# Kernel optimization log

Measured on AMD Instinct MI355X. Metric: run time of the kernel, lower is better.

The kernel has to match this reference:

```python
import jax, jax.numpy as jnp
import numpy as np

B, L, D, V = 2048, 32, 256, 100000  # batch, sentence length, embed dim, vocab
KW = 3  # kernel_width (forced to 3 by the module's shape arithmetic)


def conv_h(x, w, b):
    """1-channel conv over the seq axis, kernel (3,1), pad 2 -> length L+2. x:(B,L,D), w:(3,)."""
    xp = jnp.pad(x, ((0, 0), (2, 2), (0, 0)))
    L_out = x.shape[1] + 2
    out = w[0] * xp[:, 0:L_out] + w[1] * xp[:, 1:L_out + 1] + w[2] * xp[:, 2:L_out + 2]
    return out + b


def avgpool3(x):
    """avg_pool2d kernel (3,1) stride 1 along seq axis. (B,L+2,D) -> (B,L,D)."""
    return (x[:, :-2] + x[:, 1:-1] + x[:, 2:]) / 3.0


def conv3d_21(x, w, b):
    """Conv3d kernel (2,3,1), pad (0,2,0). x:(B,2,L,D), w:(2,3) -> (B,L+2,D)."""
    xp = jnp.pad(x, ((0, 0), (0, 0), (2, 2), (0, 0)))
    L_out = x.shape[2] + 2
    out = jnp.zeros((x.shape[0], L_out, x.shape[3]), dtype=x.dtype)
    for d0 in range(2):
        for k in range(3):
            out = out + w[d0, k] * xp[:, d0, k:k + L_out]
    return out + b


def euclid_attention(a, b):
    """A[k,i,j] = 1/(1 + ||a[k,i]-b[k,j]||_2), computed via the matmul cdist trick."""
    a2 = jnp.sum(a * a, axis=-1)  # (B,La)
    b2 = jnp.sum(b * b, axis=-1)  # (B,Lb)
    d2 = a2[:, :, None] + b2[:, None, :] - 2.0 * jnp.einsum('bid,bjd->bij', a, b)
    d = jnp.sqrt(jnp.maximum(d2, 0.0))
    return 1.0 / (1.0 + d)


def setup_inputs() -> dict:
    key = jax.random.key(0)
    ks = jax.random.split(key, 16)
    inp = {
        'sentence1': jax.random.randint(ks[0], (B, L), 0, V),
        'sentence2': jax.random.randint(ks[1], (B, L), 0, V),
        'embed': jax.random.normal(ks[2], (V, D), dtype=jnp.float32) * 0.05,
        'c1w': jax.random.normal(ks[3], (KW,), dtype=jnp.float32) * 0.3,
        'c1b': jax.random.normal(ks[4], (), dtype=jnp.float32) * 0.05,
        'c2w': jax.random.normal(ks[5], (KW,), dtype=jnp.float32) * 0.3,
        'c2b': jax.random.normal(ks[6], (), dtype=jnp.float32) * 0.05,
        'c3w': jax.random.normal(ks[7], (2, KW), dtype=jnp.float32) * 0.3,
        'c3b': jax.random.normal(ks[8], (), dtype=jnp.float32) * 0.05,
        'W0': jax.random.normal(ks[9], (L, D), dtype=jnp.float32),
        'W1': jax.random.normal(ks[10], (L, D), dtype=jnp.float32),
        'fw1': jax.random.normal(ks[11], (2 * D, 64), dtype=jnp.float32) * 0.05,
        'fb1': jnp.zeros((64,), dtype=jnp.float32),
        'fw2': jax.random.normal(ks[12], (64, 2), dtype=jnp.float32) * 0.1,
        'fb2': jnp.zeros((2,), dtype=jnp.float32),
    }
    return inp


def reference(sentence1, sentence2, embed, c1w, c1b, c2w, c2b, c3w, c3b, W0, W1, fw1, fb1, fw2, fb2):
    e1 = embed[sentence1]                      # (B,L,D)
    e2 = embed[sentence2]
    rep1 = avgpool3(conv_h(e1, c1w, c1b))      # (B,L,D)
    rep2 = avgpool3(conv_h(e2, c1w, c1b))
    A1 = euclid_attention(rep1, rep2)          # (B,L,L)
    att1 = jnp.einsum('bij,jd->bid', A1, W0)   # (B,L,D)
    att2 = jnp.einsum('bij,jd->bid', A1, W1)
    c1 = conv3d_21(jnp.stack([rep1, att1], axis=1), c3w, c3b)  # (B,L+2,D)
    c2 = conv3d_21(jnp.stack([rep2, att2], axis=1), c3w, c3b)
    A2 = euclid_attention(c1, c2)              # (B,L+2,L+2)
    col = jnp.sum(A2, axis=2)                  # (B,L+2)
    row = jnp.sum(A2, axis=1)
    ca1 = avgpool3(c1 * col[:, :, None])       # (B,L,D)
    ca2 = avgpool3(c2 * row[:, :, None])
    v1 = jnp.mean(conv_h(ca1, c2w, c2b), axis=1)  # (B,D)
    v2 = jnp.mean(conv_h(ca2, c2w, c2b), axis=1)
    h = jnp.tanh(jnp.concatenate([v1, v2], axis=1) @ fw1 + fb1)
    logits = h @ fw2 + fb2                     # (B,2)
    return jax.nn.softmax(logits, axis=0)      # faithful: original Softmax(dim=0)
```

## Files before the change

### kernel.cpp

```cpp
#include <hip/hip_runtime.h>
#include <math.h>

#define NB 2048
#define LL 32
#define DD 256
#define LP 34
#define SRH 264
#define SA 35

typedef unsigned short u16;
typedef short bf8 __attribute__((ext_vector_type(8)));
typedef float f32x4 __attribute__((ext_vector_type(4)));
typedef float vf2 __attribute__((ext_vector_type(2)));

__device__ __forceinline__ float bfu(u16 h) { return __uint_as_float(((unsigned)h) << 16); }
__device__ __forceinline__ u16 f2bf(float f) {
    unsigned u = __float_as_uint(f);
    u += 0x7fffu + ((u >> 16) & 1u);
    return (u16)(u >> 16);
}
__device__ __forceinline__ unsigned cvt_pk_bf(float lo, float hi) {
    unsigned r;
    asm("v_cvt_pk_bf16_f32 %0, %1, %2" : "=v"(r) : "v"(lo), "v"(hi));
    return r;
}

__device__ __forceinline__ f32x4 gram8(const u16* __restrict__ A, const u16* __restrict__ B) {
    f32x4 acc = {0.f, 0.f, 0.f, 0.f};
    #pragma unroll
    for (int ks = 0; ks < 8; ++ks) {
        const bf8 a = *(const bf8*)(A + ks * 32);
        const bf8 b = *(const bf8*)(B + ks * 32);
        acc = __builtin_amdgcn_mfma_f32_16x16x32_bf16(a, b, acc, 0, 0, 0);
    }
    return acc;
}

__device__ static const signed char TB2[8][4] = {
    {0,0,1,0}, {0,0,1,16}, {0,16,1,0}, {0,16,1,16},
    {0,0,0,0}, {0,16,0,16}, {1,0,1,0}, {1,16,1,16}};

__device__ static const signed char TB5[15][4] = {
    {0,0,0,0}, {0,16,0,16}, {0,18,0,18}, {1,0,1,0}, {1,16,1,16}, {1,18,1,18},
    {0,0,1,0},  {0,0,1,16},  {0,0,1,18},
    {0,16,1,0}, {0,16,1,16}, {0,16,1,18},
    {0,18,1,0}, {0,18,1,16}, {0,18,1,18}};

__global__ __launch_bounds__(256)
void pack_w(const float* __restrict__ W0, const float* __restrict__ W1, u16* __restrict__ wp)
{
    const int t = blockIdx.x * 256 + threadIdx.x;
    const int lane = t & 63, nt = (t >> 6) & 15, wsel = t >> 10;
    const float* W = wsel ? W1 : W0;
    const int col = nt * 16 + (lane & 15);
    const int k0 = (lane >> 4) * 8;
    unsigned d[4];
    #pragma unroll
    for (int q = 0; q < 4; ++q) {
        const u16 lo = f2bf(W[(size_t)(k0 + 2 * q) * DD + col]);
        const u16 hi = f2bf(W[(size_t)(k0 + 2 * q + 1) * DD + col]);
        d[q] = (unsigned)lo | ((unsigned)hi << 16);
    }
    uint4 u; u.x = d[0]; u.y = d[1]; u.z = d[2]; u.w = d[3];
    ((uint4*)wp)[t] = u;
}

__global__ __launch_bounds__(256, 4)
void abcnn_fused(const int* __restrict__ s1, const int* __restrict__ s2,
                 const float* __restrict__ embed,
                 const float* __restrict__ c1w, const float* __restrict__ c1b,
                 const float* __restrict__ c2w, const float* __restrict__ c2b,
                 const float* __restrict__ c3w, const float* __restrict__ c3b,
                 const float* __restrict__ fw1, const float* __restrict__ fb1,
                 const float* __restrict__ fw2, const float* __restrict__ fb2,
                 const u16* __restrict__ wpack, float* __restrict__ lgts)
{
    __shared__ __align__(16) u16 RC[2][LP][SRH];
    __shared__ float AU[LP * SA];
    __shared__ float nrm[2][LP];

    const int b    = blockIdx.x;
    const int tid  = threadIdx.x;
    const int lane = tid & 63;
    const int wv   = tid >> 6;
    const int c15  = lane & 15;
    const int q4x  = (lane >> 4) * 4;
    const int ko   = (lane >> 4) * 8;

    {
        const float w0 = c1w[0], w1 = c1w[1], w2 = c1w[2], bb = c1b[0];
        const float gm2 = w0 * (1.f/3.f);
        const float gm1 = (w0 + w1) * (1.f/3.f);
        const float g0  = (w0 + w1 + w2) * (1.f/3.f);
        const float gp1 = (w1 + w2) * (1.f/3.f);
        const float gp2 = w2 * (1.f/3.f);
        const int s  = __builtin_amdgcn_readfirstlane(tid >> 7);
        const int dp = tid & 127;
        const int* sent = (s ? s2 : s1) + b * LL;
        int sv[LL];
        #pragma unroll
        for (int j = 0; j < LL; ++j) sv[j] = sent[j];
        #pragma unroll
        for (int half = 0; half < 2; ++half) {
            const int j0 = half * 16;
            vf2 x[20];
            #pragma unroll
            for (int i = 0; i < 20; ++i) {
                const int rr = j0 - 2 + i;
                if (rr >= 0 && rr < LL)
                    x[i] = *(const vf2*)(embed + (size_t)sv[rr] * DD + 2 * dp);
                else
                    x[i] = (vf2){0.f, 0.f};
            }
            #pragma unroll
            for (int j = 0; j < 16; ++j) {
                vf2 acc = {bb, bb};
                acc += gm2 * x[j];
                acc += gm1 * x[j + 1];
                acc += g0  * x[j + 2];
                acc += gp1 * x[j + 3];
                acc += gp2 * x[j + 4];
                *(unsigned*)&RC[s][j0 + j][2 * dp] = cvt_pk_bf(acc.x, acc.y);
            }
        }
    }
    __syncthreads();

    {
        f32x4 h2[2];
        __builtin_amdgcn_s_setprio(1);
        #pragma unroll
        for (int k = 0; k < 2; ++k) {
            const int t  = wv * 2 + k;
            const int sa = TB2[t][0], oa = TB2[t][1], sb = TB2[t][2], ob = TB2[t][3];
            const f32x4 G = gram8(&RC[sa][oa + c15][ko], &RC[sb][ob + c15][ko]);
            h2[k] = G;
            if (t >= 4 && (c15 >> 2) == (lane >> 4)) {
                const int r = c15 & 3;
                const float dv = (r == 0) ? G[0] : (r == 1) ? G[1] : (r == 2) ? G[2] : G[3];
                nrm[sa][oa + c15] = dv;
            }
        }
        __builtin_amdgcn_s_setprio(0);
        __syncthreads();
        #pragma unroll
        for (int k = 0; k < 2; ++k) {
            const int t = wv * 2 + k;
            if (t < 4) {
                const int oa = TB2[t][1], ob = TB2[t][3];
                const f32x4 G = h2[k];
                #pragma unroll
                for (int r = 0; r < 4; ++r) {
                    const int i = oa + q4x + r, j = ob + c15;
                    const float d2 = nrm[0][i] + nrm[1][j] - 2.f * G[r];
                    AU[i * SA + j] = 1.f / (1.f + sqrtf(fmaxf(d2, 0.f)));
                }
            }
        }
    }
    __syncthreads();

    {
        const float cw10 = c3w[3], cw11 = c3w[4], cw12 = c3w[5];
        const float cw00 = c3w[0], cw01 = c3w[1], cw02 = c3w[2], cb3 = c3b[0];
        bf8 afr[3];
        #pragma unroll
        for (int rq = 0; rq < 3; ++rq) {
            const int ro = (rq == 0) ? 0 : (rq == 1) ? 16 : 18;
            const int i = ro + c15;
            bf8 af;
            #pragma unroll
            for (int j = 0; j < 8; ++j) {
                const int m = ko + j;
                float acc = 0.f;
                if (i >= 2)           acc += cw10 * AU[(i - 2) * SA + m];
                if (i >= 1 && i < 33) acc += cw11 * AU[(i - 1) * SA + m];
                if (i < 32)           acc += cw12 * AU[i * SA + m];
                af[j] = (short)f2bf(acc);
            }
            afr[rq] = af;
        }
        __builtin_amdgcn_s_setprio(1);
        #pragma unroll
        for (int wsel = 0; wsel < 2; ++wsel) {
            #pragma unroll
            for (int nidx = 0; nidx < 4; ++nidx) {
                const int n = wv + 4 * nidx;
                const int dcol = n * 16 + c15;
                const bf8 w = *(const bf8*)(wpack + (size_t)((wsel * 16 + n) * 64 + lane) * 8);
                #pragma unroll
                for (int rqd = 0; rqd < 3; ++rqd) {
                    const int rq = 2 - rqd;
                    const int ro = (rq == 0) ? 0 : (rq == 1) ? 16 : 18;
                    const int i0 = ro + q4x;
                    const f32x4 z = {0.f, 0.f, 0.f, 0.f};
                    f32x4 d4 = __builtin_amdgcn_mfma_f32_16x16x32_bf16(afr[rq], w, z, 0, 0, 0);
                    float tt[6];
                    #pragma unroll
                    for (int q2 = 0; q2 < 6; ++q2) {
                        const int rr = i0 - 2 + q2;
                        tt[q2] = (rr >= 0 && rr < LL) ? bfu(RC[wsel][rr][dcol]) : 0.f;
                    }
                    #pragma unroll
                    for (int r = 0; r < 4; ++r)
                        d4[r] += cb3 + cw00 * tt[r] + cw01 * tt[r + 1] + cw02 * tt[r + 2];
                    const unsigned p01 = cvt_pk_bf(d4[0], d4[1]);
                    const unsigned p23 = cvt_pk_bf(d4[2], d4[3]);
                    if (rq < 2) {
                        RC[wsel][i0    ][dcol] = (u16)p01;
                        RC[wsel][i0 + 1][dcol] = (u16)(p01 >> 16);
                        RC[wsel][i0 + 2][dcol] = (u16)p23;
                        RC[wsel][i0 + 3][dcol] = (u16)(p23 >> 16);
                    } else if (q4x == 12) {
                        RC[wsel][32][dcol] = (u16)p23;
                        RC[wsel][33][dcol] = (u16)(p23 >> 16);
                    }
                }
            }
        }
        __builtin_amdgcn_s_setprio(0);
    }
    __syncthreads();

    {
        f32x4 h5[4];
        __builtin_amdgcn_s_setprio(1);
        #pragma unroll
        for (int k = 0; k < 4; ++k) {
            const int t = wv + 4 * k;
            if (t < 15) {
                const int sa = TB5[t][0], oa = TB5[t][1], sb = TB5[t][2], ob = TB5[t][3];
                const f32x4 G = gram8(&RC[sa][oa + c15][ko], &RC[sb][ob + c15][ko]);
                h5[k] = G;
                if (t < 6 && (c15 >> 2) == (lane >> 4)) {
                    const int r = c15 & 3;
                    const float dv = (r == 0) ? G[0] : (r == 1) ? G[1] : (r == 2) ? G[2] : G[3];
                    nrm[sa][oa + c15] = dv;
                }
            }
        }
        __builtin_amdgcn_s_setprio(0);
        __syncthreads();
        #pragma unroll
        for (int k = 0; k < 4; ++k) {
            const int t = wv + 4 * k;
            if (t >= 6 && t < 15) {
                const int oa = TB5[t][1], ob = TB5[t][3];
                const f32x4 G = h5[k];
                #pragma unroll
                for (int r = 0; r < 4; ++r) {
                    const int i = oa + q4x + r, j = ob + c15;
                    const float d2 = nrm[0][i] + nrm[1][j] - 2.f * G[r];
                    AU[i * SA + j] = 1.f / (1.f + sqrtf(fmaxf(d2, 0.f)));
                }
            }
        }
    }
    __syncthreads();

    {
        const float S2 = c2w[0] + c2w[1] + c2w[2];
        const float sc = S2 * (1.f / 102.f);
        float p6 = 0.f;
        if (tid < 68) {
            const bool isCol = tid < 34;
            const int p = isCol ? tid : tid - 34;
            float ssum = 0.f;
            for (int q = 0; q < LP; ++q) ssum += AU[isCol ? (p * SA + q) : (q * SA + p)];
            const float cnt = (p == 0 || p == 33) ? 1.f : ((p == 1 || p == 32) ? 2.f : 3.f);
            p6 = ssum * cnt * sc;
        }
        __syncthreads();
        if (tid < 68) AU[tid] = p6;
    }
    __syncthreads();

    {
        const float cb2 = c2b[0];
        float v1 = cb2, v2 = cb2;
        #pragma unroll
        for (int p = 0; p < LP; ++p) {
            v1 += AU[p]      * bfu(RC[0][p][tid]);
            v2 += AU[34 + p] * bfu(RC[1][p][tid]);
        }
        AU[68 + tid]       = v1;
        AU[68 + 256 + tid] = v2;
    }
    __syncthreads();

    {
        const int u = tid & 63, sg = tid >> 6;
        const float* vv = &AU[68];
        const float* fp = fw1 + (size_t)(sg * 128) * 64 + u;
        float part = 0.f;
        for (int t = 0; t < 128; ++t) part += vv[sg * 128 + t] * fp[(size_t)t * 64];
        AU[580 + tid] = part;
    }
    __syncthreads();
    if (tid < 64) {
        const float hsum = AU[580 + tid] + AU[644 + tid] + AU[708 + tid] + AU[772 + tid] + fb1[tid];
        AU[836 + tid] = tanhf(hsum);
    }
    __syncthreads();
    if (tid < 2) {
        float lg = fb2[tid];
        for (int u2 = 0; u2 < 64; ++u2) lg += AU[836 + u2] * fw2[u2 * 2 + tid];
        lgts[tid * NB + b] = lg;
    }
}

__global__ __launch_bounds__(1024)
void softmax_dim0(const float* __restrict__ lgts, float* __restrict__ out)
{
    __shared__ float red[17];
    const int tid = threadIdx.x;
    for (int c = 0; c < 2; ++c) {
        const float x0 = lgts[c * NB + tid];
        const float x1 = lgts[c * NB + 1024 + tid];
        float m = fmaxf(x0, x1);
        #pragma unroll
        for (int off = 32; off >= 1; off >>= 1) m = fmaxf(m, __shfl_xor(m, off));
        if ((tid & 63) == 0) red[tid >> 6] = m;
        __syncthreads();
        if (tid == 0) { float t = red[0]; for (int i = 1; i < 16; ++i) t = fmaxf(t, red[i]); red[16] = t; }
        __syncthreads();
        m = red[16];
        const float e0 = expf(x0 - m), e1 = expf(x1 - m);
        float s = e0 + e1;
        #pragma unroll
        for (int off = 32; off >= 1; off >>= 1) s += __shfl_xor(s, off);
        if ((tid & 63) == 0) red[tid >> 6] = s;
        __syncthreads();
        if (tid == 0) { float t = 0.f; for (int i = 0; i < 16; ++i) t += red[i]; red[16] = t; }
        __syncthreads();
        const float inv = 1.f / red[16];
        out[(size_t)tid * 2 + c]          = e0 * inv;
        out[(size_t)(1024 + tid) * 2 + c] = e1 * inv;
        __syncthreads();
    }
}

extern "C" void kernel_launch(void* const* d_in, const int* in_sizes, int n_in,
                              void* d_out, int out_size, void* d_ws, size_t ws_size,
                              hipStream_t stream)
{
    (void)in_sizes; (void)n_in; (void)out_size; (void)ws_size;
    const int*   s1  = (const int*)  d_in[0];
    const int*   s2  = (const int*)  d_in[1];
    const float* emb = (const float*)d_in[2];
    const float* c1w = (const float*)d_in[3];
    const float* c1b = (const float*)d_in[4];
    const float* c2w = (const float*)d_in[5];
    const float* c2b = (const float*)d_in[6];
    const float* c3w = (const float*)d_in[7];
    const float* c3b = (const float*)d_in[8];
    const float* fw1 = (const float*)d_in[11];
    const float* fb1 = (const float*)d_in[12];
    const float* fw2 = (const float*)d_in[13];
    const float* fb2 = (const float*)d_in[14];
    const float* W0  = (const float*)d_in[9];
    const float* W1  = (const float*)d_in[10];
    u16*   wpack = (u16*)d_ws;
    float* lgts  = (float*)((char*)d_ws + 32768);
    float* out   = (float*)d_out;

    pack_w<<<dim3(8), dim3(256), 0, stream>>>(W0, W1, wpack);
    abcnn_fused<<<dim3(NB), dim3(256), 0, stream>>>(s1, s2, emb, c1w, c1b, c2w, c2b,
                                                    c3w, c3b, fw1, fb1, fw2, fb2,
                                                    wpack, lgts);
    softmax_dim0<<<dim3(1), dim3(1024), 0, stream>>>(lgts, out);
}
```

Before: 66.57 us.

## Double block to 512 threads and split each stage across eight waves

The fused per-sample kernel now launches 512 threads instead of 256, and every stage is re-partitioned so each wave does half the previous work. This covers the embedding conv halves, the gram tiles, the W0/W1 MFMA selection, the pooled reductions and the fw1 partial sums. The aim is more independent waves in flight per sample to hide gather and LDS latency, with fewer serial iterations per wave. The launch bound changes from (256,4) to (512,8), which tightens the per-thread register budget and may cause spills in the register-heavy embedding stage.

```diff
diff --git a/kernel.cpp b/kernel.cpp
--- a/kernel.cpp
+++ b/kernel.cpp
@@ -65,7 +65,7 @@
     ((uint4*)wp)[t] = u;
 }
 
-__global__ __launch_bounds__(256, 4)
+__global__ __launch_bounds__(512, 8)
 void abcnn_fused(const int* __restrict__ s1, const int* __restrict__ s2,
                  const float* __restrict__ embed,
                  const float* __restrict__ c1w, const float* __restrict__ c1b,
@@ -94,67 +94,54 @@
         const float g0  = (w0 + w1 + w2) * (1.f/3.f);
         const float gp1 = (w1 + w2) * (1.f/3.f);
         const float gp2 = w2 * (1.f/3.f);
-        const int s  = __builtin_amdgcn_readfirstlane(tid >> 7);
-        const int dp = tid & 127;
+        const int s    = __builtin_amdgcn_readfirstlane((tid >> 7) & 1);
+        const int half = __builtin_amdgcn_readfirstlane(tid >> 8);
+        const int dp   = tid & 127;
         const int* sent = (s ? s2 : s1) + b * LL;
         int sv[LL];
         #pragma unroll
         for (int j = 0; j < LL; ++j) sv[j] = sent[j];
-        #pragma unroll
-        for (int half = 0; half < 2; ++half) {
-            const int j0 = half * 16;
-            vf2 x[20];
+        const int j0 = half * 16;
+        vf2 x[20];
+        #pragma unroll
+        for (int i = 0; i < 20; ++i) {
+            const int rr = j0 - 2 + i;
+            if (rr >= 0 && rr < LL)
+                x[i] = *(const vf2*)(embed + (size_t)sv[rr] * DD + 2 * dp);
+            else
+                x[i] = (vf2){0.f, 0.f};
+        }
+        #pragma unroll
+        for (int j = 0; j < 16; ++j) {
+            vf2 acc = {bb, bb};
+            acc += gm2 * x[j];
+            acc += gm1 * x[j + 1];
+            acc += g0  * x[j + 2];
+            acc += gp1 * x[j + 3];
+            acc += gp2 * x[j + 4];
+            *(unsigned*)&RC[s][j0 + j][2 * dp] = cvt_pk_bf(acc.x, acc.y);
+        }
+    }
+    __syncthreads();
+
+    {
+        const int t  = wv;
+        const int sa = TB2[t][0], oa = TB2[t][1], sb = TB2[t][2], ob = TB2[t][3];
+        __builtin_amdgcn_s_setprio(1);
+        const f32x4 G = gram8(&RC[sa][oa + c15][ko], &RC[sb][ob + c15][ko]);
+        __builtin_amdgcn_s_setprio(0);
+        if (t >= 4 && (c15 >> 2) == (lane >> 4)) {
+            const int r = c15 & 3;
+            const float dv = (r == 0) ? G[0] : (r == 1) ? G[1] : (r == 2) ? G[2] : G[3];
+            nrm[sa][oa + c15] = dv;
+        }
+        __syncthreads();
+        if (t < 4) {
             #pragma unroll
-            for (int i = 0; i < 20; ++i) {
-                const int rr = j0 - 2 + i;
-                if (rr >= 0 && rr < LL)
-                    x[i] = *(const vf2*)(embed + (size_t)sv[rr] * DD + 2 * dp);
-                else
-                    x[i] = (vf2){0.f, 0.f};
-            }
-            #pragma unroll
-            for (int j = 0; j < 16; ++j) {
-                vf2 acc = {bb, bb};
-                acc += gm2 * x[j];
-                acc += gm1 * x[j + 1];
-                acc += g0  * x[j + 2];
-                acc += gp1 * x[j + 3];
-                acc += gp2 * x[j + 4];
-                *(unsigned*)&RC[s][j0 + j][2 * dp] = cvt_pk_bf(acc.x, acc.y);
-            }
-        }
-    }
-    __syncthreads();
-
-    {
-        f32x4 h2[2];
-        __builtin_amdgcn_s_setprio(1);
-        #pragma unroll
-        for (int k = 0; k < 2; ++k) {
-            const int t  = wv * 2 + k;
-            const int sa = TB2[t][0], oa = TB2[t][1], sb = TB2[t][2], ob = TB2[t][3];
-            const f32x4 G = gram8(&RC[sa][oa + c15][ko], &RC[sb][ob + c15][ko]);
-            h2[k] = G;
-            if (t >= 4 && (c15 >> 2) == (lane >> 4)) {
-                const int r = c15 & 3;
-                const float dv = (r == 0) ? G[0] : (r == 1) ? G[1] : (r == 2) ? G[2] : G[3];
-                nrm[sa][oa + c15] = dv;
-            }
-        }
-        __builtin_amdgcn_s_setprio(0);
-        __syncthreads();
-        #pragma unroll
-        for (int k = 0; k < 2; ++k) {
-            const int t = wv * 2 + k;
-            if (t < 4) {
-                const int oa = TB2[t][1], ob = TB2[t][3];
-                const f32x4 G = h2[k];
-                #pragma unroll
-                for (int r = 0; r < 4; ++r) {
-                    const int i = oa + q4x + r, j = ob + c15;
-                    const float d2 = nrm[0][i] + nrm[1][j] - 2.f * G[r];
-                    AU[i * SA + j] = 1.f / (1.f + sqrtf(fmaxf(d2, 0.f)));
-                }
+            for (int r = 0; r < 4; ++r) {
+                const int i = oa + q4x + r, j = ob + c15;
+                const float d2 = nrm[0][i] + nrm[1][j] - 2.f * G[r];
+                AU[i * SA + j] = 1.f / (1.f + sqrtf(fmaxf(d2, 0.f)));
             }
         }
     }
@@ -180,42 +167,41 @@
             }
             afr[rq] = af;
         }
+        const int wsel = wv >> 2;
+        const int nW   = wv & 3;
         __builtin_amdgcn_s_setprio(1);
         #pragma unroll
-        for (int wsel = 0; wsel < 2; ++wsel) {
+        for (int nidx = 0; nidx < 4; ++nidx) {
+            const int n = nW + 4 * nidx;
+            const int dcol = n * 16 + c15;
+            const bf8 w = *(const bf8*)(wpack + (size_t)((wsel * 16 + n) * 64 + lane) * 8);
             #pragma unroll
-            for (int nidx = 0; nidx < 4; ++nidx) {
-                const int n = wv + 4 * nidx;
-                const int dcol = n * 16 + c15;
-                const bf8 w = *(const bf8*)(wpack + (size_t)((wsel * 16 + n) * 64 + lane) * 8);
+            for (int rqd = 0; rqd < 3; ++rqd) {
+                const int rq = 2 - rqd;
+                const int ro = (rq == 0) ? 0 : (rq == 1) ? 16 : 18;
+                const int i0 = ro + q4x;
+                const f32x4 z = {0.f, 0.f, 0.f, 0.f};
+                f32x4 d4 = __builtin_amdgcn_mfma_f32_16x16x32_bf16(afr[rq], w, z, 0, 0, 0);
+                float tt[6];
                 #pragma unroll
-                for (int rqd = 0; rqd < 3; ++rqd) {
-                    const int rq = 2 - rqd;
-                    const int ro = (rq == 0) ? 0 : (rq == 1) ? 16 : 18;
-                    const int i0 = ro + q4x;
-                    const f32x4 z = {0.f, 0.f, 0.f, 0.f};
-                    f32x4 d4 = __builtin_amdgcn_mfma_f32_16x16x32_bf16(afr[rq], w, z, 0, 0, 0);
-                    float tt[6];
-                    #pragma unroll
-                    for (int q2 = 0; q2 < 6; ++q2) {
-                        const int rr = i0 - 2 + q2;
-                        tt[q2] = (rr >= 0 && rr < LL) ? bfu(RC[wsel][rr][dcol]) : 0.f;
-                    }
-                    #pragma unroll
-                    for (int r = 0; r < 4; ++r)
-                        d4[r] += cb3 + cw00 * tt[r] + cw01 * tt[r + 1] + cw02 * tt[r + 2];
-                    const unsigned p01 = cvt_pk_bf(d4[0], d4[1]);
-                    const unsigned p23 = cvt_pk_bf(d4[2], d4[3]);
-                    if (rq < 2) {
-                        RC[wsel][i0    ][dcol] = (u16)p01;
-                        RC[wsel][i0 + 1][dcol] = (u16)(p01 >> 16);
-                        RC[wsel][i0 + 2][dcol] = (u16)p23;
-                        RC[wsel][i0 + 3][dcol] = (u16)(p23 >> 16);
-                    } else if (q4x == 12) {
-                        RC[wsel][32][dcol] = (u16)p23;
-                        RC[wsel][33][dcol] = (u16)(p23 >> 16);
-                    }
+                for (int q2 = 0; q2 < 6; ++q2) {
+                    const int rr = i0 - 2 + q2;
+                    tt[q2] = (rr >= 0 && rr < LL) ? bfu(RC[wsel][rr][dcol]) : 0.f;
                 }
+                #pragma unroll
+                for (int r = 0; r < 4; ++r)
+                    d4[r] += cb3 + cw00 * tt[r] + cw01 * tt[r + 1] + cw02 * tt[r + 2];
+                const unsigned p01 = cvt_pk_bf(d4[0], d4[1]);
+                const unsigned p23 = cvt_pk_bf(d4[2], d4[3]);
+                if (rq < 2) {
+                    RC[wsel][i0    ][dcol] = (u16)p01;
+                    RC[wsel][i0 + 1][dcol] = (u16)(p01 >> 16);
+                    RC[wsel][i0 + 2][dcol] = (u16)p23;
+                    RC[wsel][i0 + 3][dcol] = (u16)(p23 >> 16);
+                } else if (q4x == 12) {
+                    RC[wsel][32][dcol] = (u16)p23;
+                    RC[wsel][33][dcol] = (u16)(p23 >> 16);
+                }
             }
         }
         __builtin_amdgcn_s_setprio(0);
@@ -223,11 +209,11 @@
     __syncthreads();
 
     {
-        f32x4 h5[4];
+        f32x4 h5[2];
         __builtin_amdgcn_s_setprio(1);
         #pragma unroll
-        for (int k = 0; k < 4; ++k) {
-            const int t = wv + 4 * k;
+        for (int k = 0; k < 2; ++k) {
+            const int t = wv * 2 + k;
             if (t < 15) {
                 const int sa = TB5[t][0], oa = TB5[t][1], sb = TB5[t][2], ob = TB5[t][3];
                 const f32x4 G = gram8(&RC[sa][oa + c15][ko], &RC[sb][ob + c15][ko]);
@@ -242,8 +228,8 @@
         __builtin_amdgcn_s_setprio(0);
         __syncthreads();
         #pragma unroll
-        for (int k = 0; k < 4; ++k) {
-            const int t = wv + 4 * k;
+        for (int k = 0; k < 2; ++k) {
+            const int t = wv * 2 + k;
             if (t >= 6 && t < 15) {
                 const int oa = TB5[t][1], ob = TB5[t][3];
                 const f32x4 G = h5[k];
@@ -277,34 +263,35 @@
 
     {
         const float cb2 = c2b[0];
-        float v1 = cb2, v2 = cb2;
-        #pragma unroll
-        for (int p = 0; p < LP; ++p) {
-            v1 += AU[p]      * bfu(RC[0][p][tid]);
-            v2 += AU[34 + p] * bfu(RC[1][p][tid]);
-        }
-        AU[68 + tid]       = v1;
-        AU[68 + 256 + tid] = v2;
+        const int side = tid >> 8;
+        const int d    = tid & 255;
+        float v = cb2;
+        #pragma unroll
+        for (int p = 0; p < LP; ++p)
+            v += AU[side * 34 + p] * bfu(RC[side][p][d]);
+        AU[68 + tid] = v;
     }
     __syncthreads();
 
     {
         const int u = tid & 63, sg = tid >> 6;
         const float* vv = &AU[68];
-        const float* fp = fw1 + (size_t)(sg * 128) * 64 + u;
+        const float* fp = fw1 + (size_t)(sg * 64) * 64 + u;
         float part = 0.f;
-        for (int t = 0; t < 128; ++t) part += vv[sg * 128 + t] * fp[(size_t)t * 64];
+        for (int t = 0; t < 64; ++t) part += vv[sg * 64 + t] * fp[(size_t)t * 64];
         AU[580 + tid] = part;
     }
     __syncthreads();
     if (tid < 64) {
-        const float hsum = AU[580 + tid] + AU[644 + tid] + AU[708 + tid] + AU[772 + tid] + fb1[tid];
-        AU[836 + tid] = tanhf(hsum);
+        float hsum = fb1[tid];
+        #pragma unroll
+        for (int q = 0; q < 8; ++q) hsum += AU[580 + q * 64 + tid];
+        AU[1092 + tid] = tanhf(hsum);
     }
     __syncthreads();
     if (tid < 2) {
         float lg = fb2[tid];
-        for (int u2 = 0; u2 < 64; ++u2) lg += AU[836 + u2] * fw2[u2 * 2 + tid];
+        for (int u2 = 0; u2 < 64; ++u2) lg += AU[1092 + u2] * fw2[u2 * 2 + tid];
         lgts[tid * NB + b] = lg;
     }
 }
@@ -365,7 +352,7 @@
     float* out   = (float*)d_out;
 
     pack_w<<<dim3(8), dim3(256), 0, stream>>>(W0, W1, wpack);
-    abcnn_fused<<<dim3(NB), dim3(256), 0, stream>>>(s1, s2, emb, c1w, c1b, c2w, c2b,
+    abcnn_fused<<<dim3(NB), dim3(512), 0, stream>>>(s1, s2, emb, c1w, c1b, c2w, c2b,
                                                     c3w, c3b, fw1, fb1, fw2, fb2,
                                                     wpack, lgts);
     softmax_dim0<<<dim3(1), dim3(1024), 0, stream>>>(lgts, out);
```

Measured after the change: 109.7 us. 64.7% more time.

## Process two batch items per block and prefetch next embedding gather during compute

Applied to the files above, without the earlier changes.

Each block now handles two batch items: it issues the embedding gather for the second item right after building the first item's representation, so the global loads overlap the attention, MFMA and classifier stages of the first item. The grid is halved to 1024 blocks. The cost is keeping 36 vf2 gathered values live in registers, which raises register pressure and may lower occupancy under the 4-blocks-per-CU launch bound.

```diff
diff --git a/kernel.cpp b/kernel.cpp
--- a/kernel.cpp
+++ b/kernel.cpp
@@ -65,6 +65,38 @@
     ((uint4*)wp)[t] = u;
 }
 
+__device__ __forceinline__ void gather_issue(const int* __restrict__ s1, const int* __restrict__ s2,
+                                             const float* __restrict__ embed, int b, int tid, vf2* x)
+{
+    const int s  = __builtin_amdgcn_readfirstlane(tid >> 7);
+    const int dp = tid & 127;
+    const int* sent = (s ? s2 : s1) + b * LL;
+    #pragma unroll
+    for (int i = 0; i < 36; ++i) {
+        const int rr = i - 2;
+        if (rr >= 0 && rr < LL)
+            x[i] = *(const vf2*)(embed + (size_t)sent[rr] * DD + 2 * dp);
+        else
+            x[i] = (vf2){0.f, 0.f};
+    }
+}
+
+__device__ __forceinline__ void write_rep(u16 (*RCs)[SRH], int tid, const vf2* x,
+                                          float gm2, float gm1, float g0, float gp1, float gp2, float bb)
+{
+    const int dp = tid & 127;
+    #pragma unroll
+    for (int j = 0; j < LL; ++j) {
+        vf2 acc = {bb, bb};
+        acc += gm2 * x[j];
+        acc += gm1 * x[j + 1];
+        acc += g0  * x[j + 2];
+        acc += gp1 * x[j + 3];
+        acc += gp2 * x[j + 4];
+        *(unsigned*)&RCs[j][2 * dp] = cvt_pk_bf(acc.x, acc.y);
+    }
+}
+
 __global__ __launch_bounds__(256, 4)
 void abcnn_fused(const int* __restrict__ s1, const int* __restrict__ s2,
                  const float* __restrict__ embed,
@@ -79,233 +111,214 @@
     __shared__ float AU[LP * SA];
     __shared__ float nrm[2][LP];
 
-    const int b    = blockIdx.x;
+    const int bid  = blockIdx.x;
     const int tid  = threadIdx.x;
     const int lane = tid & 63;
     const int wv   = tid >> 6;
     const int c15  = lane & 15;
     const int q4x  = (lane >> 4) * 4;
     const int ko   = (lane >> 4) * 8;
-
-    {
-        const float w0 = c1w[0], w1 = c1w[1], w2 = c1w[2], bb = c1b[0];
-        const float gm2 = w0 * (1.f/3.f);
-        const float gm1 = (w0 + w1) * (1.f/3.f);
-        const float g0  = (w0 + w1 + w2) * (1.f/3.f);
-        const float gp1 = (w1 + w2) * (1.f/3.f);
-        const float gp2 = w2 * (1.f/3.f);
-        const int s  = __builtin_amdgcn_readfirstlane(tid >> 7);
-        const int dp = tid & 127;
-        const int* sent = (s ? s2 : s1) + b * LL;
-        int sv[LL];
-        #pragma unroll
-        for (int j = 0; j < LL; ++j) sv[j] = sent[j];
-        #pragma unroll
-        for (int half = 0; half < 2; ++half) {
-            const int j0 = half * 16;
-            vf2 x[20];
-            #pragma unroll
-            for (int i = 0; i < 20; ++i) {
-                const int rr = j0 - 2 + i;
-                if (rr >= 0 && rr < LL)
-                    x[i] = *(const vf2*)(embed + (size_t)sv[rr] * DD + 2 * dp);
-                else
-                    x[i] = (vf2){0.f, 0.f};
-            }
-            #pragma unroll
-            for (int j = 0; j < 16; ++j) {
-                vf2 acc = {bb, bb};
-                acc += gm2 * x[j];
-                acc += gm1 * x[j + 1];
-                acc += g0  * x[j + 2];
-                acc += gp1 * x[j + 3];
-                acc += gp2 * x[j + 4];
-                *(unsigned*)&RC[s][j0 + j][2 * dp] = cvt_pk_bf(acc.x, acc.y);
-            }
-        }
-    }
-    __syncthreads();
-
-    {
-        f32x4 h2[2];
-        __builtin_amdgcn_s_setprio(1);
-        #pragma unroll
-        for (int k = 0; k < 2; ++k) {
-            const int t  = wv * 2 + k;
-            const int sa = TB2[t][0], oa = TB2[t][1], sb = TB2[t][2], ob = TB2[t][3];
-            const f32x4 G = gram8(&RC[sa][oa + c15][ko], &RC[sb][ob + c15][ko]);
-            h2[k] = G;
-            if (t >= 4 && (c15 >> 2) == (lane >> 4)) {
-                const int r = c15 & 3;
-                const float dv = (r == 0) ? G[0] : (r == 1) ? G[1] : (r == 2) ? G[2] : G[3];
-                nrm[sa][oa + c15] = dv;
-            }
-        }
-        __builtin_amdgcn_s_setprio(0);
-        __syncthreads();
-        #pragma unroll
-        for (int k = 0; k < 2; ++k) {
-            const int t = wv * 2 + k;
-            if (t < 4) {
-                const int oa = TB2[t][1], ob = TB2[t][3];
-                const f32x4 G = h2[k];
-                #pragma unroll
-                for (int r = 0; r < 4; ++r) {
-                    const int i = oa + q4x + r, j = ob + c15;
-                    const float d2 = nrm[0][i] + nrm[1][j] - 2.f * G[r];
-                    AU[i * SA + j] = 1.f / (1.f + sqrtf(fmaxf(d2, 0.f)));
-                }
-            }
-        }
-    }
-    __syncthreads();
-
-    {
-        const float cw10 = c3w[3], cw11 = c3w[4], cw12 = c3w[5];
-        const float cw00 = c3w[0], cw01 = c3w[1], cw02 = c3w[2], cb3 = c3b[0];
-        bf8 afr[3];
-        #pragma unroll
-        for (int rq = 0; rq < 3; ++rq) {
-            const int ro = (rq == 0) ? 0 : (rq == 1) ? 16 : 18;
-            const int i = ro + c15;
-            bf8 af;
-            #pragma unroll
-            for (int j = 0; j < 8; ++j) {
-                const int m = ko + j;
-                float acc = 0.f;
-                if (i >= 2)           acc += cw10 * AU[(i - 2) * SA + m];
-                if (i >= 1 && i < 33) acc += cw11 * AU[(i - 1) * SA + m];
-                if (i < 32)           acc += cw12 * AU[i * SA + m];
-                af[j] = (short)f2bf(acc);
-            }
-            afr[rq] = af;
-        }
-        __builtin_amdgcn_s_setprio(1);
-        #pragma unroll
-        for (int wsel = 0; wsel < 2; ++wsel) {
-            #pragma unroll
-            for (int nidx = 0; nidx < 4; ++nidx) {
-                const int n = wv + 4 * nidx;
-                const int dcol = n * 16 + c15;
-                const bf8 w = *(const bf8*)(wpack + (size_t)((wsel * 16 + n) * 64 + lane) * 8);
-                #pragma unroll
-                for (int rqd = 0; rqd < 3; ++rqd) {
-                    const int rq = 2 - rqd;
-                    const int ro = (rq == 0) ? 0 : (rq == 1) ? 16 : 18;
-                    const int i0 = ro + q4x;
-                    const f32x4 z = {0.f, 0.f, 0.f, 0.f};
-                    f32x4 d4 = __builtin_amdgcn_mfma_f32_16x16x32_bf16(afr[rq], w, z, 0, 0, 0);
-                    float tt[6];
-                    #pragma unroll
-                    for (int q2 = 0; q2 < 6; ++q2) {
-                        const int rr = i0 - 2 + q2;
-                        tt[q2] = (rr >= 0 && rr < LL) ? bfu(RC[wsel][rr][dcol]) : 0.f;
-                    }
-                    #pragma unroll
-                    for (int r = 0; r < 4; ++r)
-                        d4[r] += cb3 + cw00 * tt[r] + cw01 * tt[r + 1] + cw02 * tt[r + 2];
-                    const unsigned p01 = cvt_pk_bf(d4[0], d4[1]);
-                    const unsigned p23 = cvt_pk_bf(d4[2], d4[3]);
-                    if (rq < 2) {
-                        RC[wsel][i0    ][dcol] = (u16)p01;
-                        RC[wsel][i0 + 1][dcol] = (u16)(p01 >> 16);
-                        RC[wsel][i0 + 2][dcol] = (u16)p23;
-                        RC[wsel][i0 + 3][dcol] = (u16)(p23 >> 16);
-                    } else if (q4x == 12) {
-                        RC[wsel][32][dcol] = (u16)p23;
-                        RC[wsel][33][dcol] = (u16)(p23 >> 16);
-                    }
-                }
-            }
-        }
-        __builtin_amdgcn_s_setprio(0);
-    }
-    __syncthreads();
-
-    {
-        f32x4 h5[4];
-        __builtin_amdgcn_s_setprio(1);
-        #pragma unroll
-        for (int k = 0; k < 4; ++k) {
-            const int t = wv + 4 * k;
-            if (t < 15) {
-                const int sa = TB5[t][0], oa = TB5[t][1], sb = TB5[t][2], ob = TB5[t][3];
+    const int sSel = __builtin_amdgcn_readfirstlane(tid >> 7);
+
+    const float w0 = c1w[0], w1 = c1w[1], w2 = c1w[2], bb = c1b[0];
+    const float gm2 = w0 * (1.f/3.f);
+    const float gm1 = (w0 + w1) * (1.f/3.f);
+    const float g0  = (w0 + w1 + w2) * (1.f/3.f);
+    const float gp1 = (w1 + w2) * (1.f/3.f);
+    const float gp2 = w2 * (1.f/3.f);
+
+    vf2 x[36];
+    gather_issue(s1, s2, embed, bid, tid, x);
+
+    for (int bi = 0; bi < 2; ++bi) {
+        const int b = bid + bi * 1024;
+
+        write_rep(RC[sSel], tid, x, gm2, gm1, g0, gp1, gp2, bb);
+        __syncthreads();
+        if (bi == 0)
+            gather_issue(s1, s2, embed, bid + 1024, tid, x);
+
+        {
+            f32x4 h2[2];
+            __builtin_amdgcn_s_setprio(1);
+            #pragma unroll
+            for (int k = 0; k < 2; ++k) {
+                const int t  = wv * 2 + k;
+                const int sa = TB2[t][0], oa = TB2[t][1], sb = TB2[t][2], ob = TB2[t][3];
                 const f32x4 G = gram8(&RC[sa][oa + c15][ko], &RC[sb][ob + c15][ko]);
-                h5[k] = G;
-                if (t < 6 && (c15 >> 2) == (lane >> 4)) {
+                h2[k] = G;
+                if (t >= 4 && (c15 >> 2) == (lane >> 4)) {
                     const int r = c15 & 3;
                     const float dv = (r == 0) ? G[0] : (r == 1) ? G[1] : (r == 2) ? G[2] : G[3];
                     nrm[sa][oa + c15] = dv;
                 }
             }
-        }
-        __builtin_amdgcn_s_setprio(0);
-        __syncthreads();
-        #pragma unroll
-        for (int k = 0; k < 4; ++k) {
-            const int t = wv + 4 * k;
-            if (t >= 6 && t < 15) {
-                const int oa = TB5[t][1], ob = TB5[t][3];
-                const f32x4 G = h5[k];
+            __builtin_amdgcn_s_setprio(0);
+            __syncthreads();
+            #pragma unroll
+            for (int k = 0; k < 2; ++k) {
+                const int t = wv * 2 + k;
+                if (t < 4) {
+                    const int oa = TB2[t][1], ob = TB2[t][3];
+                    const f32x4 G = h2[k];
+                    #pragma unroll
+                    for (int r = 0; r < 4; ++r) {
+                        const int i = oa + q4x + r, j = ob + c15;
+                        const float d2 = nrm[0][i] + nrm[1][j] - 2.f * G[r];
+                        AU[i * SA + j] = 1.f / (1.f + sqrtf(fmaxf(d2, 0.f)));
+                    }
+                }
+            }
+        }
+        __syncthreads();
+
+        {
+            const float cw10 = c3w[3], cw11 = c3w[4], cw12 = c3w[5];
+            const float cw00 = c3w[0], cw01 = c3w[1], cw02 = c3w[2], cb3 = c3b[0];
+            bf8 afr[3];
+            #pragma unroll
+            for (int rq = 0; rq < 3; ++rq) {
+                const int ro = (rq == 0) ? 0 : (rq == 1) ? 16 : 18;
+                const int i = ro + c15;
+                bf8 af;
                 #pragma unroll
-                for (int r = 0; r < 4; ++r) {
-                    const int i = oa + q4x + r, j = ob + c15;
-                    const float d2 = nrm[0][i] + nrm[1][j] - 2.f * G[r];
-                    AU[i * SA + j] = 1.f / (1.f + sqrtf(fmaxf(d2, 0.f)));
-                }
-            }
-        }
-    }
-    __syncthreads();
-
-    {
-        const float S2 = c2w[0] + c2w[1] + c2w[2];
-        const float sc = S2 * (1.f / 102.f);
-        float p6 = 0.f;
-        if (tid < 68) {
-            const bool isCol = tid < 34;
-            const int p = isCol ? tid : tid - 34;
-            float ssum = 0.f;
-            for (int q = 0; q < LP; ++q) ssum += AU[isCol ? (p * SA + q) : (q * SA + p)];
-            const float cnt = (p == 0 || p == 33) ? 1.f : ((p == 1 || p == 32) ? 2.f : 3.f);
-            p6 = ssum * cnt * sc;
-        }
-        __syncthreads();
-        if (tid < 68) AU[tid] = p6;
-    }
-    __syncthreads();
-
-    {
-        const float cb2 = c2b[0];
-        float v1 = cb2, v2 = cb2;
-        #pragma unroll
-        for (int p = 0; p < LP; ++p) {
-            v1 += AU[p]      * bfu(RC[0][p][tid]);
-            v2 += AU[34 + p] * bfu(RC[1][p][tid]);
-        }
-        AU[68 + tid]       = v1;
-        AU[68 + 256 + tid] = v2;
-    }
-    __syncthreads();
-
-    {
-        const int u = tid & 63, sg = tid >> 6;
-        const float* vv = &AU[68];
-        const float* fp = fw1 + (size_t)(sg * 128) * 64 + u;
-        float part = 0.f;
-        for (int t = 0; t < 128; ++t) part += vv[sg * 128 + t] * fp[(size_t)t * 64];
-        AU[580 + tid] = part;
-    }
-    __syncthreads();
-    if (tid < 64) {
-        const float hsum = AU[580 + tid] + AU[644 + tid] + AU[708 + tid] + AU[772 + tid] + fb1[tid];
-        AU[836 + tid] = tanhf(hsum);
-    }
-    __syncthreads();
-    if (tid < 2) {
-        float lg = fb2[tid];
-        for (int u2 = 0; u2 < 64; ++u2) lg += AU[836 + u2] * fw2[u2 * 2 + tid];
-        lgts[tid * NB + b] = lg;
+                for (int j = 0; j < 8; ++j) {
+                    const int m = ko + j;
+                    float acc = 0.f;
+                    if (i >= 2)           acc += cw10 * AU[(i - 2) * SA + m];
+                    if (i >= 1 && i < 33) acc += cw11 * AU[(i - 1) * SA + m];
+                    if (i < 32)           acc += cw12 * AU[i * SA + m];
+                    af[j] = (short)f2bf(acc);
+                }
+                afr[rq] = af;
+            }
+            __builtin_amdgcn_s_setprio(1);
+            #pragma unroll
+            for (int wsel = 0; wsel < 2; ++wsel) {
+                #pragma unroll
+                for (int nidx = 0; nidx < 4; ++nidx) {
+                    const int n = wv + 4 * nidx;
+                    const int dcol = n * 16 + c15;
+                    const bf8 w = *(const bf8*)(wpack + (size_t)((wsel * 16 + n) * 64 + lane) * 8);
+                    #pragma unroll
+                    for (int rqd = 0; rqd < 3; ++rqd) {
+                        const int rq = 2 - rqd;
+                        const int ro = (rq == 0) ? 0 : (rq == 1) ? 16 : 18;
+                        const int i0 = ro + q4x;
+                        const f32x4 z = {0.f, 0.f, 0.f, 0.f};
+                        f32x4 d4 = __builtin_amdgcn_mfma_f32_16x16x32_bf16(afr[rq], w, z, 0, 0, 0);
+                        float tt[6];
+                        #pragma unroll
+                        for (int q2 = 0; q2 < 6; ++q2) {
+                            const int rr = i0 - 2 + q2;
+                            tt[q2] = (rr >= 0 && rr < LL) ? bfu(RC[wsel][rr][dcol]) : 0.f;
+                        }
+                        #pragma unroll
+                        for (int r = 0; r < 4; ++r)
+                            d4[r] += cb3 + cw00 * tt[r] + cw01 * tt[r + 1] + cw02 * tt[r + 2];
+                        const unsigned p01 = cvt_pk_bf(d4[0], d4[1]);
+                        const unsigned p23 = cvt_pk_bf(d4[2], d4[3]);
+                        if (rq < 2) {
+                            RC[wsel][i0    ][dcol] = (u16)p01;
+                            RC[wsel][i0 + 1][dcol] = (u16)(p01 >> 16);
+                            RC[wsel][i0 + 2][dcol] = (u16)p23;
+                            RC[wsel][i0 + 3][dcol] = (u16)(p23 >> 16);
+                        } else if (q4x == 12) {
+                            RC[wsel][32][dcol] = (u16)p23;
+                            RC[wsel][33][dcol] = (u16)(p23 >> 16);
+                        }
+                    }
+                }
+            }
+            __builtin_amdgcn_s_setprio(0);
+        }
+        __syncthreads();
+
+        {
+            f32x4 h5[4];
+            __builtin_amdgcn_s_setprio(1);
+            #pragma unroll
+            for (int k = 0; k < 4; ++k) {
+                const int t = wv + 4 * k;
+                if (t < 15) {
+                    const int sa = TB5[t][0], oa = TB5[t][1], sb = TB5[t][2], ob = TB5[t][3];
+                    const f32x4 G = gram8(&RC[sa][oa + c15][ko], &RC[sb][ob + c15][ko]);
+                    h5[k] = G;
+                    if (t < 6 && (c15 >> 2) == (lane >> 4)) {
+                        const int r = c15 & 3;
+                        const float dv = (r == 0) ? G[0] : (r == 1) ? G[1] : (r == 2) ? G[2] : G[3];
+                        nrm[sa][oa + c15] = dv;
+                    }
+                }
+            }
+            __builtin_amdgcn_s_setprio(0);
+            __syncthreads();
+            #pragma unroll
+            for (int k = 0; k < 4; ++k) {
+                const int t = wv + 4 * k;
+                if (t >= 6 && t < 15) {
+                    const int oa = TB5[t][1], ob = TB5[t][3];
+                    const f32x4 G = h5[k];
+                    #pragma unroll
+                    for (int r = 0; r < 4; ++r) {
+                        const int i = oa + q4x + r, j = ob + c15;
+                        const float d2 = nrm[0][i] + nrm[1][j] - 2.f * G[r];
+                        AU[i * SA + j] = 1.f / (1.f + sqrtf(fmaxf(d2, 0.f)));
+                    }
+                }
+            }
+        }
+        __syncthreads();
+
+        {
+            const float S2 = c2w[0] + c2w[1] + c2w[2];
+            const float sc = S2 * (1.f / 102.f);
+            float p6 = 0.f;
+            if (tid < 68) {
+                const bool isCol = tid < 34;
+                const int p = isCol ? tid : tid - 34;
+                float ssum = 0.f;
+                for (int q = 0; q < LP; ++q) ssum += AU[isCol ? (p * SA + q) : (q * SA + p)];
+                const float cnt = (p == 0 || p == 33) ? 1.f : ((p == 1 || p == 32) ? 2.f : 3.f);
+                p6 = ssum * cnt * sc;
+            }
+            __syncthreads();
+            if (tid < 68) AU[tid] = p6;
+        }
+        __syncthreads();
+
+        {
+            const float cb2 = c2b[0];
+            float v1 = cb2, v2 = cb2;
+            #pragma unroll
+            for (int p = 0; p < LP; ++p) {
+                v1 += AU[p]      * bfu(RC[0][p][tid]);
+                v2 += AU[34 + p] * bfu(RC[1][p][tid]);
+            }
+            AU[68 + tid]       = v1;
+            AU[68 + 256 + tid] = v2;
+        }
+        __syncthreads();
+
+        {
+            const int u = tid & 63, sg = tid >> 6;
+            const float* vv = &AU[68];
+            const float* fp = fw1 + (size_t)(sg * 128) * 64 + u;
+            float part = 0.f;
+            for (int t = 0; t < 128; ++t) part += vv[sg * 128 + t] * fp[(size_t)t * 64];
+            AU[580 + tid] = part;
+        }
+        __syncthreads();
+        if (tid < 64) {
+            const float hsum = AU[580 + tid] + AU[644 + tid] + AU[708 + tid] + AU[772 + tid] + fb1[tid];
+            AU[836 + tid] = tanhf(hsum);
+        }
+        __syncthreads();
+        if (tid < 2) {
+            float lg = fb2[tid];
+            for (int u2 = 0; u2 < 64; ++u2) lg += AU[836 + u2] * fw2[u2 * 2 + tid];
+            lgts[tid * NB + b] = lg;
+        }
     }
 }
 
@@ -365,8 +378,8 @@
     float* out   = (float*)d_out;
 
     pack_w<<<dim3(8), dim3(256), 0, stream>>>(W0, W1, wpack);
-    abcnn_fused<<<dim3(NB), dim3(256), 0, stream>>>(s1, s2, emb, c1w, c1b, c2w, c2b,
-                                                    c3w, c3b, fw1, fb1, fw2, fb2,
-                                                    wpack, lgts);
+    abcnn_fused<<<dim3(1024), dim3(256), 0, stream>>>(s1, s2, emb, c1w, c1b, c2w, c2b,
+                                                      c3w, c3b, fw1, fb1, fw2, fb2,
+                                                      wpack, lgts);
     softmax_dim0<<<dim3(1), dim3(1024), 0, stream>>>(lgts, out);
 }
```

Result: slower. 199.0 us (+198.9%).
